# Performance work log

Hardware: AMD Instinct MI355X
Metric: run time of the kernel (lower is better)

Reference implementation:

```python
import jax, jax.numpy as jnp
import numpy as np

EPS = 1e-6

def _sigma(x):
    # ELU+1 feature map used by Infini-Attention / linear attention
    return jax.nn.elu(x) + 1.0

def setup_inputs() -> dict:
    key = jax.random.key(0)
    ks = jax.random.split(key, 8)
    B, S, H, D = 2, 4096, 2048, 128
    sc = 1.0 / np.sqrt(H)
    return {
        "hidden_states": jax.random.normal(ks[0], (B, S, H), jnp.float32),
        "w_q": jax.random.normal(ks[1], (D, H), jnp.float32) * sc,
        "w_k": jax.random.normal(ks[2], (D, H), jnp.float32) * sc,
        "w_v": jax.random.normal(ks[3], (D, H), jnp.float32) * sc,
        "w_o": jax.random.normal(ks[4], (H, D), jnp.float32) * (1.0 / np.sqrt(D)),
        "gate": jnp.zeros((1,), jnp.float32),
        "M": jax.random.normal(ks[5], (D, D), jnp.float32),
        "z": jax.random.uniform(ks[6], (D,), jnp.float32) + 0.5,
    }

def reference(hidden_states, w_q, w_k, w_v, w_o, gate, M, z):
    # projections (torch Linear: x @ W^T)
    q = jnp.einsum('bsh,dh->bsd', hidden_states, w_q)
    k = jnp.einsum('bsh,dh->bsd', hidden_states, w_k)
    v = jnp.einsum('bsh,dh->bsd', hidden_states, w_v)

    # --- compressive memory retrieve: sigma(q) M / (sigma(q) . z) ---
    sq = _sigma(q)                                   # [B,S,D]
    mem_num = jnp.einsum('bsd,de->bse', sq, M)       # [B,S,D]
    mem_den = jnp.einsum('bsd,d->bs', sq, z) + EPS
    memory_output = mem_num / mem_den[..., None]

    # --- causal linear attention (cumulative-sum, non-softmax) ---
    pq, pk = _sigma(q), _sigma(k)
    kv_cum = jnp.cumsum(jnp.einsum('bsd,bse->bsde', pk, v), axis=1)  # [B,S,D,D] running state
    k_cum = jnp.cumsum(pk, axis=1)                                    # [B,S,D]
    num = jnp.einsum('bsd,bsde->bse', pq, kv_cum)
    den = jnp.einsum('bsd,bsd->bs', pq, k_cum) + EPS
    local_output = num / den[..., None]

    g = jax.nn.sigmoid(gate)                         # [1], broadcasts
    output = g * memory_output + (1.0 - g) * local_output

    # --- delta-rule memory update ---
    sk = _sigma(k)
    v_ret = jnp.einsum('bsd,de->bse', sk, M) / (jnp.einsum('bsd,d->bs', sk, z) + EPS)[..., None]
    M_new = M + jnp.einsum('bsd,bse->de', sk, v - v_ret)
    z_new = z + jnp.sum(sk, axis=(0, 1))

    out = jnp.einsum('bsd,hd->bsh', output, w_o)
    return out, M_new, z_new
```

## Files before the change

kernel.cpp:

```cpp
#include <hip/hip_runtime.h>
#include <hip/hip_bf16.h>
#include <math.h>

#define DI __device__ __forceinline__

typedef __bf16 bf16x8 __attribute__((ext_vector_type(8)));
typedef float  f32x4  __attribute__((ext_vector_type(4)));

static constexpr int   Bsz  = 2, Ssz = 4096, Hsz = 2048, Dsz = 128;
static constexpr int   Nrow = Bsz * Ssz;
static constexpr int   NCH  = Nrow / 128;
static constexpr int   CPB  = Ssz / 128;
static constexpr int   WN   = Dsz * Hsz;
static constexpr float EPSF = 1e-6f;

static constexpr size_t WQKV_OFF = 0;
static constexpr size_t WO_OFF   = (size_t)3*WN*2;
static constexpr size_t MB_OFF   = WO_OFF + (size_t)WN*2;
static constexpr size_t MBT_OFF  = MB_OFF + 32768;
static constexpr size_t QB_OFF   = MBT_OFF + 32768;
static constexpr size_t KB_OFF   = QB_OFF + (size_t)Nrow*Dsz*2;
static constexpr size_t VB_OFF   = KB_OFF + (size_t)Nrow*Dsz*2;
static constexpr size_t PB_OFF   = VB_OFF + (size_t)Nrow*Dsz*2;
static constexpr size_t ACC_OFF  = PB_OFF + (size_t)Nrow*Dsz*2;
static constexpr size_t KV_OFF   = ACC_OFF;
static constexpr size_t KVP_OFF  = ACC_OFF + (size_t)4*1024*1024;
static constexpr size_t MPART_OFF= ACC_OFF + (size_t)6*1024*1024;
static constexpr size_t KSUM_OFF = ACC_OFF + (size_t)10*1024*1024;
static constexpr size_t KPRE_OFF = KSUM_OFF + 32768;

DI float b2f(unsigned short u) {
    union { float f; unsigned int i; } x; x.i = ((unsigned int)u) << 16; return x.f;
}
DI unsigned short f2b(float f) {
    __bf16 h = (__bf16)f; return __builtin_bit_cast(unsigned short, h);
}
DI float sig_elu(float x) { return x > 0.f ? x + 1.f : expf(x); }

DI f32x4 MFMA(bf16x8 a, bf16x8 b, f32x4 c) {
    return __builtin_amdgcn_mfma_f32_16x16x32_bf16(a, b, c, 0, 0, 0);
}
template<int NB>
DI void zaccg(f32x4 (&acc)[4][NB]) {
    f32x4 zz = {0.f, 0.f, 0.f, 0.f};
    #pragma unroll
    for (int i = 0; i < 4; i++)
        #pragma unroll
        for (int j = 0; j < NB; j++) acc[i][j] = zz;
}

DI void gll16(const void* g, void* l) {
    __builtin_amdgcn_global_load_lds((const __attribute__((address_space(1))) void*)g,
                                     (__attribute__((address_space(3))) void*)l, 16, 0, 0);
}

DI int swzR(int r, int kc, int R) { return (kc*R + (r ^ (kc & 7))) * 8; }

template<int NKS, int NB>
DI void mmg(const unsigned short* A, const unsigned short* Bm, f32x4 (&acc)[4][NB],
            int wm, int wn, int quad, int lr) {
    #pragma unroll
    for (int ks = 0; ks < NKS; ks++) {
        bf16x8 a[4], b[NB];
        #pragma unroll
        for (int mb = 0; mb < 4; mb++)
            a[mb] = *(const bf16x8*)&A[swzR(wm*64 + mb*16 + lr, ks*4 + quad, 128)];
        #pragma unroll
        for (int nb = 0; nb < NB; nb++)
            b[nb] = *(const bf16x8*)&Bm[swzR(wn*(NB*16) + nb*16 + lr, ks*4 + quad, NB*32)];
        #pragma unroll
        for (int mb = 0; mb < 4; mb++)
            #pragma unroll
            for (int nb = 0; nb < NB; nb++)
                acc[mb][nb] = MFMA(a[mb], b[nb], acc[mb][nb]);
    }
}

template<int R>
DI void stage_dir(unsigned short* dst, const unsigned short* src, int src_ld, int tid) {
    #pragma unroll
    for (int i = 0; i < R/16; i++) {
        int s = tid + i*256; int r = s >> 4, kc = s & 15;
        *(uint4*)&dst[swzR(r, kc, R)] = *(const uint4*)(src + (size_t)r*src_ld + kc*8);
    }
}

DI void stage_T128(unsigned short* dst, const unsigned short* src, int src_ld, int tid) {
    #pragma unroll
    for (int i = 0; i < 8; i++) {
        int s = tid + i*256;
        int rw = (s & 15) + ((s >> 8) << 4);
        int c0 = ((s >> 4) & 15) * 8;
        unsigned short tmp[8];
        *(uint4*)tmp = *(const uint4*)(src + (size_t)rw*src_ld + c0);
        #pragma unroll
        for (int j = 0; j < 8; j++)
            dst[swzR(c0 + j, rw >> 3, 128) + (rw & 7)] = tmp[j];
    }
}

DI void stage_T32(unsigned short* dst, const unsigned short* src, int src_ld, int colOff, int tid) {
    #pragma unroll
    for (int i = 0; i < 2; i++) {
        int s = tid + i*256;
        int rw = (s & 15) + ((s >> 6) << 4);
        int c0 = ((s >> 4) & 3) * 8;
        unsigned short tmp[8];
        *(uint4*)tmp = *(const uint4*)(src + (size_t)rw*src_ld + colOff + c0);
        #pragma unroll
        for (int j = 0; j < 8; j++)
            dst[swzR(c0 + j, rw >> 3, 32) + (rw & 7)] = tmp[j];
    }
}


__global__ void k_cvt_w(const float* __restrict__ wq, const float* __restrict__ wk,
                        const float* __restrict__ wv, const float* __restrict__ wo,
                        const float* __restrict__ M, unsigned short* __restrict__ dst,
                        unsigned short* __restrict__ MbT)
{
    int gid = blockIdx.x*256 + threadIdx.x;
    if (gid >= (4*WN + 16384)/4) return;
    int e = gid*4;
    const float* src; int rel;
    if      (e < WN)     { src = wq; rel = e; }
    else if (e < 2*WN)   { src = wk; rel = e - WN; }
    else if (e < 3*WN)   { src = wv; rel = e - 2*WN; }
    else if (e < 4*WN)   { src = wo; rel = e - 3*WN; }
    else                 { src = M;  rel = e - 4*WN; }
    float4 v = *(const float4*)(src + rel);
    const float* vf = (const float*)&v;
    unsigned short o[4];
    #pragma unroll
    for (int j = 0; j < 4; j++) o[j] = f2b(vf[j]);
    *(uint2*)&dst[e] = *(const uint2*)o;
    if (e >= 4*WN) {
        #pragma unroll
        for (int j = 0; j < 4; j++) {
            int d = (rel + j) >> 7, ee = (rel + j) & 127;
            MbT[ee*128 + d] = o[j];
        }
    }
}

__global__ __launch_bounds__(512, 2) void k_gemm_qkv(
    const float* __restrict__ X, const unsigned short* __restrict__ W,
    unsigned short* __restrict__ AccB)
{
    __shared__ unsigned short lA[128*64];
    __shared__ unsigned short lB[384*64];
    const int tid = threadIdx.x;
    const int row0 = blockIdx.x * 128;
    const int kb   = blockIdx.y * 512;
    const int wave = tid >> 6, lane = tid & 63;
    const int wm = wave >> 2, wn = wave & 3;
    const int quad = lane >> 4, lr = lane & 15;

    const int cA0 = tid, cA1 = tid + 512;
    const int rA0 = cA0 >> 3, kA0 = cA0 & 7;
    const int rA1 = cA1 >> 3, kA1 = cA1 & 7;
    const float* pA0 = X + (size_t)(row0 + rA0)*Hsz + kA0*8;
    const float* pA1 = X + (size_t)(row0 + rA1)*Hsz + kA1*8;
    unsigned short* wA0 = &lA[(rA0*8 + (kA0 ^ (rA0 & 7)))*8];
    unsigned short* wA1 = &lA[(rA1*8 + (kA1 ^ (rA1 & 7)))*8];

    f32x4 acc[4][6];
    {
        f32x4 zz = {0.f, 0.f, 0.f, 0.f};
        #pragma unroll
        for (int i = 0; i < 4; i++)
            #pragma unroll
            for (int j = 0; j < 6; j++) acc[i][j] = zz;
    }

    float4 a00 = *(const float4*)(pA0 + kb);
    float4 a01 = *(const float4*)(pA0 + kb + 4);
    float4 a10 = *(const float4*)(pA1 + kb);
    float4 a11 = *(const float4*)(pA1 + kb + 4);

    for (int kt = kb; kt < kb + 512; kt += 64) {
        #pragma unroll
        for (int i = 0; i < 6; i++) {
            int p = tid + i*512; int r = p >> 3; int kc = (p & 7) ^ (r & 7);
            gll16(W + (size_t)r*Hsz + kt + kc*8, &lB[p*8]);
        }
        {
            unsigned short o[8];
            const float* f0 = (const float*)&a00; const float* f1 = (const float*)&a01;
            #pragma unroll
            for (int j = 0; j < 4; j++) { o[j] = f2b(f0[j]); o[4+j] = f2b(f1[j]); }
            *(uint4*)wA0 = *(const uint4*)o;
            const float* f2 = (const float*)&a10; const float* f3 = (const float*)&a11;
            #pragma unroll
            for (int j = 0; j < 4; j++) { o[j] = f2b(f2[j]); o[4+j] = f2b(f3[j]); }
            *(uint4*)wA1 = *(const uint4*)o;
        }
        __syncthreads();
        if (kt + 64 < kb + 512) {
            a00 = *(const float4*)(pA0 + kt + 64);
            a01 = *(const float4*)(pA0 + kt + 64 + 4);
            a10 = *(const float4*)(pA1 + kt + 64);
            a11 = *(const float4*)(pA1 + kt + 64 + 4);
        }
        #pragma unroll
        for (int ks = 0; ks < 2; ks++) {
            bf16x8 a[4], b[6];
            #pragma unroll
            for (int mb = 0; mb < 4; mb++) {
                int r = wm*64 + mb*16 + lr;
                int c = (ks*4 + quad) ^ (r & 7);
                a[mb] = *(const bf16x8*)&lA[(r*8 + c)*8];
            }
            #pragma unroll
            for (int nb = 0; nb < 6; nb++) {
                int r = wn*96 + nb*16 + lr;
                int c = (ks*4 + quad) ^ (r & 7);
                b[nb] = *(const bf16x8*)&lB[(r*8 + c)*8];
            }
            #pragma unroll
            for (int mb = 0; mb < 4; mb++)
                #pragma unroll
                for (int nb = 0; nb < 6; nb++)
                    acc[mb][nb] = MFMA(a[mb], b[nb], acc[mb][nb]);
        }
        __syncthreads();
    }

    unsigned short* base = AccB + (size_t)blockIdx.y * 3 * Nrow * 128;
    #pragma unroll
    for (int mb = 0; mb < 4; mb++)
        #pragma unroll
        for (int nb = 0; nb < 6; nb++)
            #pragma unroll
            for (int rg = 0; rg < 4; rg++) {
                int s_ = wm*64 + mb*16 + quad*4 + rg;
                int n  = wn*96 + nb*16 + lr;
                int ct = n >> 7, e_ = n & 127;
                base[(size_t)ct*Nrow*128 + (size_t)(row0 + s_)*128 + e_] =
                    f2b(acc[mb][nb][rg]);
            }
}

__global__ void k_qkv_epi(const unsigned short* __restrict__ AccB,
                          unsigned short* __restrict__ Qb,
                          unsigned short* __restrict__ Kb, unsigned short* __restrict__ Vb)
{
    int gid = blockIdx.x*256 + threadIdx.x;
    int ct = gid / (Nrow*16);
    int off = (gid - ct*Nrow*16) * 8;
    float vs[8];
    #pragma unroll
    for (int j = 0; j < 8; j++) vs[j] = 0.f;
    #pragma unroll
    for (int s = 0; s < 4; s++) {
        uint4 u = *(const uint4*)&AccB[((size_t)s*3 + ct)*Nrow*128 + off];
        const unsigned short* us = (const unsigned short*)&u;
        #pragma unroll
        for (int j = 0; j < 8; j++) vs[j] += b2f(us[j]);
    }
    unsigned short o[8];
    if (ct < 2) {
        #pragma unroll
        for (int j = 0; j < 8; j++) o[j] = f2b(sig_elu(vs[j]));
    } else {
        #pragma unroll
        for (int j = 0; j < 8; j++) o[j] = f2b(vs[j]);
    }
    unsigned short* dst = (ct == 0) ? Qb : (ct == 1 ? Kb : Vb);
    *(uint4*)&dst[off] = *(const uint4*)o;
}

__global__ __launch_bounds__(256, 2) void k_delta_kv(
    const unsigned short* __restrict__ Kb, const unsigned short* __restrict__ Vb,
    const unsigned short* __restrict__ MbT, const float* __restrict__ z,
    float* __restrict__ KV, float* __restrict__ ksum, float* __restrict__ Mpart)
{
    __shared__ unsigned short b0[128*128];
    __shared__ unsigned short b1a[32*128];
    __shared__ unsigned short b1b[32*128];
    __shared__ unsigned short b1c[32*128];
    __shared__ float den[128];
    const int tid = threadIdx.x;
    const int c = blockIdx.x, t0 = c*128;
    const int e0 = blockIdx.y * 32;
    const int wave = tid >> 6, lane = tid & 63;
    const int wm = wave >> 1, wn = wave & 1, quad = lane >> 4, lr = lane & 15;

    stage_dir<128>(b0, Kb + (size_t)t0*Dsz, Dsz, tid);
    stage_dir<32>(b1a, MbT + (size_t)e0*128, 128, tid);
    __syncthreads();

    f32x4 acc1[4][1]; zaccg(acc1);
    mmg<4,1>(b0, b1a, acc1, wm, wn, quad, lr);

    if (tid < 128) {
        float p = 0.f;
        for (int d = 0; d < 128; d++)
            p += b2f(b0[swzR(tid, d >> 3, 128) + (d & 7)]) * z[d];
        den[tid] = p + EPSF;
    }
    __syncthreads();

    stage_T128(b0, Kb + (size_t)t0*Dsz, Dsz, tid);
    stage_T32(b1c, Vb + (size_t)t0*Dsz, Dsz, e0, tid);
    #pragma unroll
    for (int mb = 0; mb < 4; mb++)
        #pragma unroll
        for (int rg = 0; rg < 4; rg++) {
            int s_ = wm*64 + mb*16 + quad*4 + rg;
            int el = wn*16 + lr;
            float v = b2f(Vb[(size_t)(t0 + s_)*Dsz + e0 + el]);
            float w = v - acc1[mb][0][rg] / den[s_];
            b1b[swzR(el, s_ >> 3, 32) + (s_ & 7)] = f2b(w);
        }
    __syncthreads();

    if (e0 == 0 && tid < 128) {
        float p = 0.f;
        for (int t = 0; t < 128; t++)
            p += b2f(b0[swzR(tid, t >> 3, 128) + (t & 7)]);
        ksum[(size_t)c*128 + tid] = p;
    }
    f32x4 acc2[4][1]; zaccg(acc2);
    mmg<4,1>(b0, b1b, acc2, wm, wn, quad, lr);
    f32x4 acc3[4][1]; zaccg(acc3);
    mmg<4,1>(b0, b1c, acc3, wm, wn, quad, lr);
    #pragma unroll
    for (int mb = 0; mb < 4; mb++)
        #pragma unroll
        for (int rg = 0; rg < 4; rg++) {
            int d_ = wm*64 + mb*16 + quad*4 + rg;
            int el = wn*16 + lr;
            Mpart[(size_t)c*16384 + (size_t)d_*128 + e0 + el] = acc2[mb][0][rg];
            KV[(size_t)c*16384 + (size_t)d_*128 + e0 + el]    = acc3[mb][0][rg];
        }
}

__global__ void k_scan_final(
    const float* __restrict__ KV, const float* __restrict__ ksum,
    const float* __restrict__ M, const float* __restrict__ z,
    const float* __restrict__ Mpart, unsigned short* __restrict__ KVp,
    float* __restrict__ kpre, float* __restrict__ omz)
{
    int idx = blockIdx.x*256 + threadIdx.x;
    if (idx < 32768) {
        int batch = idx >> 14, ed = idx & 16383;
        float a = 0.f;
        #pragma unroll 8
        for (int i = 0; i < CPB; i++) {
            size_t cc = (size_t)(batch*CPB + i);
            KVp[cc*16384 + ed] = f2b(a);
            a += KV[cc*16384 + ed];
        }
    } else if (idx < 33024) {
        int j = idx - 32768; int batch = j >> 7, d = j & 127;
        float a = 0.f;
        #pragma unroll 8
        for (int i = 0; i < CPB; i++) {
            int cc = batch*CPB + i;
            kpre[cc*128 + d] = a;
            a += ksum[cc*128 + d];
        }
    } else if (idx < 49408) {
        int m = idx - 33024;
        float a = M[m];
        #pragma unroll 8
        for (int cc = 0; cc < NCH; cc++) a += Mpart[(size_t)cc*16384 + m];
        omz[m] = a;
    } else if (idx < 49536) {
        int d = idx - 49408;
        float a = z[d];
        #pragma unroll 8
        for (int cc = 0; cc < NCH; cc++) a += ksum[cc*128 + d];
        omz[16384 + d] = a;
    }
}

__global__ __launch_bounds__(256, 2) void k_attn(
    const unsigned short* __restrict__ Qb, const unsigned short* __restrict__ KVp,
    const float* __restrict__ kpre, const unsigned short* __restrict__ MbT,
    const float* __restrict__ z, const float* __restrict__ gate,
    const unsigned short* __restrict__ Kb, const unsigned short* __restrict__ Vb,
    unsigned short* __restrict__ P)
{
    __shared__ unsigned short b0[128*128];
    __shared__ unsigned short b1[128*128];
    __shared__ float dmem[128], dl[128], rs[128];
    const int tid = threadIdx.x;
    const int c = blockIdx.x, t0 = c*128;
    const int e0 = blockIdx.y * 32;
    const int wave = tid >> 6, lane = tid & 63;
    const int wm = wave >> 1, wn = wave & 1, quad = lane >> 4, lr = lane & 15;
    unsigned short* b1q0 = b1;
    unsigned short* b1q1 = b1 + 32*128;

    if (tid < 128) rs[tid] = 0.f;
    stage_dir<128>(b0, Qb + (size_t)t0*Dsz, Dsz, tid);
    stage_dir<32>(b1q0, MbT + (size_t)e0*128, 128, tid);
    stage_T32(b1q1, KVp + (size_t)c*16384, 128, e0, tid);
    __syncthreads();

    if (tid < 128) {
        float p = 0.f;
        for (int d = 0; d < 128; d++)
            p += b2f(b0[swzR(tid, d >> 3, 128) + (d & 7)]) * z[d];
        dmem[tid] = p + EPSF;
    } else {
        int s_ = tid - 128; float p = 0.f;
        for (int d = 0; d < 128; d++)
            p += b2f(b0[swzR(s_, d >> 3, 128) + (d & 7)]) * kpre[c*128 + d];
        dl[s_] = p;
    }
    f32x4 accM[4][1]; zaccg(accM);
    mmg<4,1>(b0, b1q0, accM, wm, wn, quad, lr);
    f32x4 accN[4][1]; zaccg(accN);
    mmg<4,1>(b0, b1q1, accN, wm, wn, quad, lr);
    __syncthreads();

    float g = 1.f / (1.f + expf(-gate[0]));
    f32x4 base[4][1];
    #pragma unroll
    for (int mb = 0; mb < 4; mb++)
        #pragma unroll
        for (int rg = 0; rg < 4; rg++) {
            int s_ = wm*64 + mb*16 + quad*4 + rg;
            base[mb][0][rg] = g * accM[mb][0][rg] / dmem[s_];
        }
    stage_dir<128>(b1, Kb + (size_t)t0*Dsz, Dsz, tid);
    __syncthreads();

    f32x4 accS[4][4]; zaccg(accS);
    mmg<4,4>(b0, b1, accS, wm, wn, quad, lr);
    __syncthreads();

    #pragma unroll
    for (int mb = 0; mb < 4; mb++)
        #pragma unroll
        for (int rg = 0; rg < 4; rg++) {
            int s_ = wm*64 + mb*16 + quad*4 + rg;
            float part = 0.f;
            #pragma unroll
            for (int nb = 0; nb < 4; nb++) {
                int t_ = wn*64 + nb*16 + lr;
                float v = (t_ <= s_) ? accS[mb][nb][rg] : 0.f;
                part += v;
                b0[swzR(s_, t_ >> 3, 128) + (t_ & 7)] = f2b(v);
            }
            #pragma unroll
            for (int m = 1; m < 16; m <<= 1) part += __shfl_xor(part, m, 64);
            if (lr == 0) atomicAdd(&rs[s_], part);
        }
    stage_T32(b1q0, Vb + (size_t)t0*Dsz, Dsz, e0, tid);
    __syncthreads();

    f32x4 accV[4][1]; zaccg(accV);
    mmg<4,1>(b0, b1q0, accV, wm, wn, quad, lr);

    #pragma unroll
    for (int mb = 0; mb < 4; mb++)
        #pragma unroll
        for (int rg = 0; rg < 4; rg++) {
            int s_ = wm*64 + mb*16 + quad*4 + rg;
            int el = wn*16 + lr;
            float num = accN[mb][0][rg] + accV[mb][0][rg];
            float dd  = dl[s_] + rs[s_] + EPSF;
            float val = base[mb][0][rg] + (1.f - g) * num / dd;
            P[(size_t)(t0 + s_)*Dsz + e0 + el] = f2b(val);
        }
}

__global__ __launch_bounds__(256, 2) void k_gemm_out(
    const unsigned short* __restrict__ P, const unsigned short* __restrict__ Wo,
    float* __restrict__ out)
{
    __shared__ unsigned short b0[128*128];
    __shared__ unsigned short b1[128*128];
    const int tid = threadIdx.x;
    const int row0 = blockIdx.x*128, n0 = blockIdx.y*128;
    const int wave = tid >> 6, lane = tid & 63;
    const int wm = wave >> 1, wn = wave & 1, quad = lane >> 4, lr = lane & 15;

    #pragma unroll
    for (int i = 0; i < 8; i++) {
        int p = tid + i*256; int r = p >> 4; int kc = (p & 15) ^ (r & 15);
        gll16(P + (size_t)(row0 + r)*Dsz + kc*8, &b0[p*8]);
    }
    #pragma unroll
    for (int i = 0; i < 8; i++) {
        int p = tid + i*256; int r = p >> 4; int kc = (p & 15) ^ (r & 15);
        gll16(Wo + (size_t)(n0 + r)*Dsz + kc*8, &b1[p*8]);
    }
    __syncthreads();

    f32x4 acc[4][4]; zaccg(acc);
    #pragma unroll
    for (int ks = 0; ks < 4; ks++) {
        bf16x8 a[4], b[4];
        #pragma unroll
        for (int mb = 0; mb < 4; mb++) {
            int r = wm*64 + mb*16 + lr;
            a[mb] = *(const bf16x8*)&b0[(r*16 + ((ks*4 + quad) ^ (r & 15)))*8];
        }
        #pragma unroll
        for (int nb = 0; nb < 4; nb++) {
            int r = wn*64 + nb*16 + lr;
            b[nb] = *(const bf16x8*)&b1[(r*16 + ((ks*4 + quad) ^ (r & 15)))*8];
        }
        #pragma unroll
        for (int mb = 0; mb < 4; mb++)
            #pragma unroll
            for (int nb = 0; nb < 4; nb++)
                acc[mb][nb] = MFMA(a[mb], b[nb], acc[mb][nb]);
    }
    #pragma unroll
    for (int mb = 0; mb < 4; mb++)
        #pragma unroll
        for (int nb = 0; nb < 4; nb++)
            #pragma unroll
            for (int rg = 0; rg < 4; rg++) {
                int s_ = wm*64 + mb*16 + quad*4 + rg;
                int e_ = wn*64 + nb*16 + lr;
                out[(size_t)(row0 + s_)*Hsz + n0 + e_] = acc[mb][nb][rg];
            }
}

extern "C" void kernel_launch(void* const* d_in, const int* in_sizes, int n_in,
                              void* d_out, int out_size, void* d_ws, size_t ws_size,
                              hipStream_t stream)
{
    const float* X    = (const float*)d_in[0];
    const float* wq   = (const float*)d_in[1];
    const float* wk   = (const float*)d_in[2];
    const float* wv   = (const float*)d_in[3];
    const float* wo   = (const float*)d_in[4];
    const float* gate = (const float*)d_in[5];
    const float* M    = (const float*)d_in[6];
    const float* z    = (const float*)d_in[7];

    char* ws = (char*)d_ws;
    unsigned short* Wfull = (unsigned short*)(ws + WQKV_OFF);
    unsigned short* Wo_b  = (unsigned short*)(ws + WO_OFF);
    unsigned short* MbT   = (unsigned short*)(ws + MBT_OFF);
    unsigned short* Qb    = (unsigned short*)(ws + QB_OFF);
    unsigned short* Kb    = (unsigned short*)(ws + KB_OFF);
    unsigned short* Vb    = (unsigned short*)(ws + VB_OFF);
    unsigned short* Pb    = (unsigned short*)(ws + PB_OFF);
    unsigned short* AccB  = (unsigned short*)(ws + ACC_OFF);
    float* KV    = (float*)(ws + KV_OFF);
    unsigned short* KVp = (unsigned short*)(ws + KVP_OFF);
    float* Mpart = (float*)(ws + MPART_OFF);
    float* ksum  = (float*)(ws + KSUM_OFF);
    float* kpre  = (float*)(ws + KPRE_OFF);

    float* outp   = (float*)d_out;
    float* out_mz = outp + (size_t)Nrow*Hsz;

    k_cvt_w<<<((4*WN + 16384)/4 + 255)/256, 256, 0, stream>>>(wq, wk, wv, wo, M, Wfull, MbT);
    k_gemm_qkv<<<dim3(Nrow/128, 4), 512, 0, stream>>>(X, Wfull, AccB);
    k_qkv_epi<<<(3*Nrow*16)/256, 256, 0, stream>>>(AccB, Qb, Kb, Vb);
    k_delta_kv<<<dim3(NCH, 4), 256, 0, stream>>>(Kb, Vb, MbT, z, KV, ksum, Mpart);
    k_scan_final<<<194, 256, 0, stream>>>(KV, ksum, M, z, Mpart, KVp, kpre, out_mz);
    k_attn<<<dim3(NCH, 4), 256, 0, stream>>>(Qb, KVp, kpre, MbT, z, gate, Kb, Vb, Pb);
    k_gemm_out<<<dim3(Nrow/128, Hsz/128), 256, 0, stream>>>(Pb, Wo_b, outp);
}
```

Baseline: 180.2 us.

## Split delta-KV and attention kernels across a z-dimension to double block count

The delta_kv and attn kernels now launch twice as many blocks via a z grid dimension. In delta_kv, each block computes half of the d rows for the Mpart and KV outputs. In attn, each block handles 64 of the 128 query rows, and the lower half uses a reduced causal key range. This targets low occupancy: only 256 blocks ran per kernel before. The cost is duplicated staging of K and the acc1 delta-rule projection in each half, and delta_kv now uses more shared memory.

```diff
diff --git a/kernel.cpp b/kernel.cpp
--- a/kernel.cpp
+++ b/kernel.cpp
@@ -48,6 +48,14 @@
         #pragma unroll
         for (int j = 0; j < NB; j++) acc[i][j] = zz;
 }
+template<int NB>
+DI void zacc2(f32x4 (&acc)[2][NB]) {
+    f32x4 zz = {0.f, 0.f, 0.f, 0.f};
+    #pragma unroll
+    for (int i = 0; i < 2; i++)
+        #pragma unroll
+        for (int j = 0; j < NB; j++) acc[i][j] = zz;
+}
 
 DI void gll16(const void* g, void* l) {
     __builtin_amdgcn_global_load_lds((const __attribute__((address_space(1))) void*)g,
@@ -70,6 +78,26 @@
             b[nb] = *(const bf16x8*)&Bm[swzR(wn*(NB*16) + nb*16 + lr, ks*4 + quad, NB*32)];
         #pragma unroll
         for (int mb = 0; mb < 4; mb++)
+            #pragma unroll
+            for (int nb = 0; nb < NB; nb++)
+                acc[mb][nb] = MFMA(a[mb], b[nb], acc[mb][nb]);
+    }
+}
+
+template<int NKS, int NB>
+DI void mmg64(const unsigned short* A, const unsigned short* Bm, f32x4 (&acc)[2][NB],
+              int wm, int wn, int quad, int lr) {
+    #pragma unroll
+    for (int ks = 0; ks < NKS; ks++) {
+        bf16x8 a[2], b[NB];
+        #pragma unroll
+        for (int mb = 0; mb < 2; mb++)
+            a[mb] = *(const bf16x8*)&A[swzR(wm*32 + mb*16 + lr, ks*4 + quad, 64)];
+        #pragma unroll
+        for (int nb = 0; nb < NB; nb++)
+            b[nb] = *(const bf16x8*)&Bm[swzR(wn*(NB*16) + nb*16 + lr, ks*4 + quad, NB*32)];
+        #pragma unroll
+        for (int mb = 0; mb < 2; mb++)
             #pragma unroll
             for (int nb = 0; nb < NB; nb++)
                 acc[mb][nb] = MFMA(a[mb], b[nb], acc[mb][nb]);
@@ -96,6 +124,20 @@
         #pragma unroll
         for (int j = 0; j < 8; j++)
             dst[swzR(c0 + j, rw >> 3, 128) + (rw & 7)] = tmp[j];
+    }
+}
+
+DI void stage_T64(unsigned short* dst, const unsigned short* src, int src_ld, int colOff, int tid) {
+    #pragma unroll
+    for (int i = 0; i < 4; i++) {
+        int s = tid + i*256;
+        int rw = s >> 3;
+        int c0 = (s & 7) * 8;
+        unsigned short tmp[8];
+        *(uint4*)tmp = *(const uint4*)(src + (size_t)rw*src_ld + colOff + c0);
+        #pragma unroll
+        for (int j = 0; j < 8; j++)
+            dst[swzR(c0 + j, rw >> 3, 64) + (rw & 7)] = tmp[j];
     }
 }
 
@@ -276,6 +318,7 @@
     float* __restrict__ KV, float* __restrict__ ksum, float* __restrict__ Mpart)
 {
     __shared__ unsigned short b0[128*128];
+    __shared__ unsigned short bA[64*128];
     __shared__ unsigned short b1a[32*128];
     __shared__ unsigned short b1b[32*128];
     __shared__ unsigned short b1c[32*128];
@@ -283,11 +326,14 @@
     const int tid = threadIdx.x;
     const int c = blockIdx.x, t0 = c*128;
     const int e0 = blockIdx.y * 32;
+    const int dh = blockIdx.z;
     const int wave = tid >> 6, lane = tid & 63;
     const int wm = wave >> 1, wn = wave & 1, quad = lane >> 4, lr = lane & 15;
 
     stage_dir<128>(b0, Kb + (size_t)t0*Dsz, Dsz, tid);
+    stage_T64(bA, Kb + (size_t)t0*Dsz, Dsz, dh*64, tid);
     stage_dir<32>(b1a, MbT + (size_t)e0*128, 128, tid);
+    stage_T32(b1c, Vb + (size_t)t0*Dsz, Dsz, e0, tid);
     __syncthreads();
 
     f32x4 acc1[4][1]; zaccg(acc1);
@@ -298,11 +344,15 @@
         for (int d = 0; d < 128; d++)
             p += b2f(b0[swzR(tid, d >> 3, 128) + (d & 7)]) * z[d];
         den[tid] = p + EPSF;
+        if (e0 == 0 && dh == 0) {
+            float q = 0.f;
+            for (int t = 0; t < 128; t++)
+                q += b2f(b0[swzR(t, tid >> 3, 128) + (tid & 7)]);
+            ksum[(size_t)c*128 + tid] = q;
+        }
     }
     __syncthreads();
 
-    stage_T128(b0, Kb + (size_t)t0*Dsz, Dsz, tid);
-    stage_T32(b1c, Vb + (size_t)t0*Dsz, Dsz, e0, tid);
     #pragma unroll
     for (int mb = 0; mb < 4; mb++)
         #pragma unroll
@@ -315,21 +365,15 @@
         }
     __syncthreads();
 
-    if (e0 == 0 && tid < 128) {
-        float p = 0.f;
-        for (int t = 0; t < 128; t++)
-            p += b2f(b0[swzR(tid, t >> 3, 128) + (t & 7)]);
-        ksum[(size_t)c*128 + tid] = p;
-    }
-    f32x4 acc2[4][1]; zaccg(acc2);
-    mmg<4,1>(b0, b1b, acc2, wm, wn, quad, lr);
-    f32x4 acc3[4][1]; zaccg(acc3);
-    mmg<4,1>(b0, b1c, acc3, wm, wn, quad, lr);
-    #pragma unroll
-    for (int mb = 0; mb < 4; mb++)
+    f32x4 acc2[2][1]; zacc2(acc2);
+    mmg64<4,1>(bA, b1b, acc2, wm, wn, quad, lr);
+    f32x4 acc3[2][1]; zacc2(acc3);
+    mmg64<4,1>(bA, b1c, acc3, wm, wn, quad, lr);
+    #pragma unroll
+    for (int mb = 0; mb < 2; mb++)
         #pragma unroll
         for (int rg = 0; rg < 4; rg++) {
-            int d_ = wm*64 + mb*16 + quad*4 + rg;
+            int d_ = dh*64 + wm*32 + mb*16 + quad*4 + rg;
             int el = wn*16 + lr;
             Mpart[(size_t)c*16384 + (size_t)d_*128 + e0 + el] = acc2[mb][0][rg];
             KV[(size_t)c*16384 + (size_t)d_*128 + e0 + el]    = acc3[mb][0][rg];
@@ -376,6 +420,109 @@
     }
 }
 
+template<int H>
+DI void attn_impl(const unsigned short* Qb, const unsigned short* KVp,
+                  const float* kpre, const unsigned short* MbT,
+                  const float* z, const float* gate,
+                  const unsigned short* Kb, const unsigned short* Vb,
+                  unsigned short* P,
+                  unsigned short* b0q, unsigned short* b1,
+                  unsigned short* bq0, unsigned short* bq1,
+                  float* dmem, float* dl, float* rs,
+                  int c, int e0, int tid)
+{
+    const int t0 = c*128;
+    const int wave = tid >> 6, lane = tid & 63;
+    const int wm = wave >> 1, wn = wave & 1, quad = lane >> 4, lr = lane & 15;
+    constexpr int NBT = H ? 4 : 2;
+    constexpr int NKV = H ? 4 : 2;
+
+    if (tid < 64) rs[tid] = 0.f;
+    stage_dir<64>(b0q, Qb + (size_t)(t0 + H*64)*Dsz, Dsz, tid);
+    stage_dir<128>(b1, Kb + (size_t)t0*Dsz, Dsz, tid);
+    stage_dir<32>(bq0, MbT + (size_t)e0*128, 128, tid);
+    stage_T32(bq1, KVp + (size_t)c*16384, 128, e0, tid);
+    __syncthreads();
+
+    if (tid < 64) {
+        float p = 0.f;
+        for (int d = 0; d < 128; d++)
+            p += b2f(b0q[swzR(tid, d >> 3, 64) + (d & 7)]) * z[d];
+        dmem[tid] = p + EPSF;
+    } else if (tid < 128) {
+        int s_ = tid - 64; float p = 0.f;
+        for (int d = 0; d < 128; d++)
+            p += b2f(b0q[swzR(s_, d >> 3, 64) + (d & 7)]) * kpre[c*128 + d];
+        dl[s_] = p;
+    }
+    f32x4 accM[2][1]; zacc2(accM);
+    mmg64<4,1>(b0q, bq0, accM, wm, wn, quad, lr);
+    f32x4 accN[2][1]; zacc2(accN);
+    mmg64<4,1>(b0q, bq1, accN, wm, wn, quad, lr);
+    f32x4 accS[2][NBT]; zacc2(accS);
+    #pragma unroll
+    for (int ks = 0; ks < 4; ks++) {
+        bf16x8 a[2], b[NBT];
+        #pragma unroll
+        for (int mb = 0; mb < 2; mb++)
+            a[mb] = *(const bf16x8*)&b0q[swzR(wm*32 + mb*16 + lr, ks*4 + quad, 64)];
+        #pragma unroll
+        for (int nb = 0; nb < NBT; nb++)
+            b[nb] = *(const bf16x8*)&b1[swzR(wn*(NBT*16) + nb*16 + lr, ks*4 + quad, 128)];
+        #pragma unroll
+        for (int mb = 0; mb < 2; mb++)
+            #pragma unroll
+            for (int nb = 0; nb < NBT; nb++)
+                accS[mb][nb] = MFMA(a[mb], b[nb], accS[mb][nb]);
+    }
+    __syncthreads();
+
+    float g = 1.f / (1.f + expf(-gate[0]));
+    f32x4 base[2][1];
+    #pragma unroll
+    for (int mb = 0; mb < 2; mb++)
+        #pragma unroll
+        for (int rg = 0; rg < 4; rg++) {
+            int s_ = wm*32 + mb*16 + quad*4 + rg;
+            base[mb][0][rg] = g * accM[mb][0][rg] / dmem[s_];
+        }
+    #pragma unroll
+    for (int mb = 0; mb < 2; mb++)
+        #pragma unroll
+        for (int rg = 0; rg < 4; rg++) {
+            int s_ = wm*32 + mb*16 + quad*4 + rg;
+            int sa = H*64 + s_;
+            float part = 0.f;
+            #pragma unroll
+            for (int nb = 0; nb < NBT; nb++) {
+                int t_ = wn*(NBT*16) + nb*16 + lr;
+                float v = (t_ <= sa) ? accS[mb][nb][rg] : 0.f;
+                part += v;
+                b1[swzR(s_, t_ >> 3, 64) + (t_ & 7)] = f2b(v);
+            }
+            #pragma unroll
+            for (int m = 1; m < 16; m <<= 1) part += __shfl_xor(part, m, 64);
+            if (lr == 0) atomicAdd(&rs[s_], part);
+        }
+    stage_T32(bq0, Vb + (size_t)t0*Dsz, Dsz, e0, tid);
+    __syncthreads();
+
+    f32x4 accV[2][1]; zacc2(accV);
+    mmg64<NKV,1>(b1, bq0, accV, wm, wn, quad, lr);
+
+    #pragma unroll
+    for (int mb = 0; mb < 2; mb++)
+        #pragma unroll
+        for (int rg = 0; rg < 4; rg++) {
+            int s_ = wm*32 + mb*16 + quad*4 + rg;
+            int el = wn*16 + lr;
+            float num = accN[mb][0][rg] + accV[mb][0][rg];
+            float dd  = dl[s_] + rs[s_] + EPSF;
+            float val = base[mb][0][rg] + (1.f - g) * num / dd;
+            P[(size_t)(t0 + H*64 + s_)*Dsz + e0 + el] = f2b(val);
+        }
+}
+
 __global__ __launch_bounds__(256, 2) void k_attn(
     const unsigned short* __restrict__ Qb, const unsigned short* __restrict__ KVp,
     const float* __restrict__ kpre, const unsigned short* __restrict__ MbT,
@@ -383,90 +530,18 @@
     const unsigned short* __restrict__ Kb, const unsigned short* __restrict__ Vb,
     unsigned short* __restrict__ P)
 {
-    __shared__ unsigned short b0[128*128];
+    __shared__ unsigned short b0q[64*128];
     __shared__ unsigned short b1[128*128];
-    __shared__ float dmem[128], dl[128], rs[128];
-    const int tid = threadIdx.x;
-    const int c = blockIdx.x, t0 = c*128;
-    const int e0 = blockIdx.y * 32;
-    const int wave = tid >> 6, lane = tid & 63;
-    const int wm = wave >> 1, wn = wave & 1, quad = lane >> 4, lr = lane & 15;
-    unsigned short* b1q0 = b1;
-    unsigned short* b1q1 = b1 + 32*128;
-
-    if (tid < 128) rs[tid] = 0.f;
-    stage_dir<128>(b0, Qb + (size_t)t0*Dsz, Dsz, tid);
-    stage_dir<32>(b1q0, MbT + (size_t)e0*128, 128, tid);
-    stage_T32(b1q1, KVp + (size_t)c*16384, 128, e0, tid);
-    __syncthreads();
-
-    if (tid < 128) {
-        float p = 0.f;
-        for (int d = 0; d < 128; d++)
-            p += b2f(b0[swzR(tid, d >> 3, 128) + (d & 7)]) * z[d];
-        dmem[tid] = p + EPSF;
-    } else {
-        int s_ = tid - 128; float p = 0.f;
-        for (int d = 0; d < 128; d++)
-            p += b2f(b0[swzR(s_, d >> 3, 128) + (d & 7)]) * kpre[c*128 + d];
-        dl[s_] = p;
-    }
-    f32x4 accM[4][1]; zaccg(accM);
-    mmg<4,1>(b0, b1q0, accM, wm, wn, quad, lr);
-    f32x4 accN[4][1]; zaccg(accN);
-    mmg<4,1>(b0, b1q1, accN, wm, wn, quad, lr);
-    __syncthreads();
-
-    float g = 1.f / (1.f + expf(-gate[0]));
-    f32x4 base[4][1];
-    #pragma unroll
-    for (int mb = 0; mb < 4; mb++)
-        #pragma unroll
-        for (int rg = 0; rg < 4; rg++) {
-            int s_ = wm*64 + mb*16 + quad*4 + rg;
-            base[mb][0][rg] = g * accM[mb][0][rg] / dmem[s_];
-        }
-    stage_dir<128>(b1, Kb + (size_t)t0*Dsz, Dsz, tid);
-    __syncthreads();
-
-    f32x4 accS[4][4]; zaccg(accS);
-    mmg<4,4>(b0, b1, accS, wm, wn, quad, lr);
-    __syncthreads();
-
-    #pragma unroll
-    for (int mb = 0; mb < 4; mb++)
-        #pragma unroll
-        for (int rg = 0; rg < 4; rg++) {
-            int s_ = wm*64 + mb*16 + quad*4 + rg;
-            float part = 0.f;
-            #pragma unroll
-            for (int nb = 0; nb < 4; nb++) {
-                int t_ = wn*64 + nb*16 + lr;
-                float v = (t_ <= s_) ? accS[mb][nb][rg] : 0.f;
-                part += v;
-                b0[swzR(s_, t_ >> 3, 128) + (t_ & 7)] = f2b(v);
-            }
-            #pragma unroll
-            for (int m = 1; m < 16; m <<= 1) part += __shfl_xor(part, m, 64);
-            if (lr == 0) atomicAdd(&rs[s_], part);
-        }
-    stage_T32(b1q0, Vb + (size_t)t0*Dsz, Dsz, e0, tid);
-    __syncthreads();
-
-    f32x4 accV[4][1]; zaccg(accV);
-    mmg<4,1>(b0, b1q0, accV, wm, wn, quad, lr);
-
-    #pragma unroll
-    for (int mb = 0; mb < 4; mb++)
-        #pragma unroll
-        for (int rg = 0; rg < 4; rg++) {
-            int s_ = wm*64 + mb*16 + quad*4 + rg;
-            int el = wn*16 + lr;
-            float num = accN[mb][0][rg] + accV[mb][0][rg];
-            float dd  = dl[s_] + rs[s_] + EPSF;
-            float val = base[mb][0][rg] + (1.f - g) * num / dd;
-            P[(size_t)(t0 + s_)*Dsz + e0 + el] = f2b(val);
-        }
+    __shared__ unsigned short bq0[32*128];
+    __shared__ unsigned short bq1[32*128];
+    __shared__ float dmem[64], dl[64], rs[64];
+    const int c = blockIdx.x, e0 = blockIdx.y * 32, tid = threadIdx.x;
+    if (blockIdx.z == 0)
+        attn_impl<0>(Qb, KVp, kpre, MbT, z, gate, Kb, Vb, P,
+                     b0q, b1, bq0, bq1, dmem, dl, rs, c, e0, tid);
+    else
+        attn_impl<1>(Qb, KVp, kpre, MbT, z, gate, Kb, Vb, P,
+                     b0q, b1, bq0, bq1, dmem, dl, rs, c, e0, tid);
 }
 
 __global__ __launch_bounds__(256, 2) void k_gemm_out(
@@ -558,8 +633,8 @@
     k_cvt_w<<<((4*WN + 16384)/4 + 255)/256, 256, 0, stream>>>(wq, wk, wv, wo, M, Wfull, MbT);
     k_gemm_qkv<<<dim3(Nrow/128, 4), 512, 0, stream>>>(X, Wfull, AccB);
     k_qkv_epi<<<(3*Nrow*16)/256, 256, 0, stream>>>(AccB, Qb, Kb, Vb);
-    k_delta_kv<<<dim3(NCH, 4), 256, 0, stream>>>(Kb, Vb, MbT, z, KV, ksum, Mpart);
+    k_delta_kv<<<dim3(NCH, 4, 2), 256, 0, stream>>>(Kb, Vb, MbT, z, KV, ksum, Mpart);
     k_scan_final<<<194, 256, 0, stream>>>(KV, ksum, M, z, Mpart, KVp, kpre, out_mz);
-    k_attn<<<dim3(NCH, 4), 256, 0, stream>>>(Qb, KVp, kpre, MbT, z, gate, Kb, Vb, Pb);
+    k_attn<<<dim3(NCH, 4, 2), 256, 0, stream>>>(Qb, KVp, kpre, MbT, z, gate, Kb, Vb, Pb);
     k_gemm_out<<<dim3(Nrow/128, Hsz/128), 256, 0, stream>>>(Pb, Wo_b, outp);
 }
```

Result: no change. 178.6 us (-0.9%).
